# Kernel tuning notes

Hardware: AMD Instinct MI355X
Metric: run time of the kernel (lower is better)

## Reference

```python
import jax, jax.numpy as jnp
import numpy as np

N_WIN = 7
NUM_HEADS = 8
DIM = 256
QK = 256
TOPK = 4
MLP_HID = 4 * DIM
SCALE = QK ** -0.5  # used for both region routing and pixel attention (qk_scale=None)


def _layernorm(x, g, b, eps=1e-6):
    mu = jnp.mean(x, axis=-1, keepdims=True)
    var = jnp.mean(jnp.square(x - mu), axis=-1, keepdims=True)
    return (x - mu) * jax.lax.rsqrt(var + eps) * g + b


def _dwconv(x, w, b):
    # x: NHWC, w: (5,5,1,C) depthwise kernel (torch Conv2d groups=C, padding=2)
    y = jax.lax.conv_general_dilated(
        x, w, window_strides=(1, 1), padding='SAME',
        feature_group_count=x.shape[-1],
        dimension_numbers=('NHWC', 'HWIO', 'NHWC'))
    return y + b


def _bra(x, qkv_w, qkv_b, lepe_w, lepe_b, wo_w, wo_b):
    # BiLevelRoutingAttention, NHWC in/out
    N, H, W, C = x.shape
    j = i = N_WIN
    h, w = H // j, W // i
    p2, w2, m = j * i, h * w, NUM_HEADS
    dq, dv = QK // m, C // m
    # window partition: (N, p2, h, w, C)
    xw = x.reshape(N, j, h, i, w, C).transpose(0, 1, 3, 2, 4, 5).reshape(N, p2, h, w, C)
    qkv = xw @ qkv_w + qkv_b
    q = qkv[..., :QK]            # (N,p2,h,w,QK)
    kv = qkv[..., QK:]           # (N,p2,h,w,QK+C)
    q_pix = q.reshape(N, p2, w2, QK)
    kv_pix = kv.reshape(N, p2, w2, QK + C)
    q_win = jnp.mean(q, axis=(2, 3))                    # (N,p2,QK)
    k_win = jnp.mean(kv[..., :QK], axis=(2, 3))         # (N,p2,QK)
    # LePE: depthwise conv on V in full-image layout
    v_img = kv[..., QK:].reshape(N, j, i, h, w, C).transpose(0, 1, 3, 2, 4, 5).reshape(N, H, W, C)
    lepe = _dwconv(v_img, lepe_w, lepe_b)
    # region-to-region routing, top-k window selection
    logit = jnp.einsum('npc,nqc->npq', q_win * SCALE, k_win)    # (N,p2,p2)
    _, r_idx = jax.lax.top_k(logit, TOPK)                       # (N,p2,TOPK)
    # gather KV of selected windows: (N,p2,TOPK,w2,QK+C)
    kv_sel = kv_pix[jnp.arange(N)[:, None, None], r_idx]
    k_sel = kv_sel[..., :QK].reshape(N, p2, TOPK * w2, m, dq).transpose(0, 1, 3, 2, 4)  # (N,p2,m,kw2,dq)
    v_sel = kv_sel[..., QK:].reshape(N, p2, TOPK * w2, m, dv).transpose(0, 1, 3, 2, 4)  # (N,p2,m,kw2,dv)
    q_h = q_pix.reshape(N, p2, w2, m, dq).transpose(0, 1, 3, 2, 4)                      # (N,p2,m,w2,dq)
    aw = jnp.einsum('npmqd,npmkd->npmqk', q_h * SCALE, k_sel)
    aw = jax.nn.softmax(aw, axis=-1)
    out = jnp.einsum('npmqk,npmkd->npmqd', aw, v_sel)           # (N,p2,m,w2,dv)
    out = out.transpose(0, 1, 3, 2, 4).reshape(N, j, i, h, w, C)
    out = out.transpose(0, 1, 3, 2, 4, 5).reshape(N, H, W, C)
    out = out + lepe
    return out @ wo_w + wo_b


def setup_inputs() -> dict:
    key = jax.random.key(0)
    ks = jax.random.split(key, 8)
    s = 0.02
    return {
        'x': jax.random.normal(ks[0], (8, 56, 56, DIM), dtype=jnp.float32),
        'ln1_g': jnp.ones((DIM,), jnp.float32),
        'ln1_b': jnp.zeros((DIM,), jnp.float32),
        'qkv_w': jax.random.normal(ks[1], (DIM, 2 * QK + DIM), jnp.float32) * s,
        'qkv_b': jnp.zeros((2 * QK + DIM,), jnp.float32),
        'lepe_w': jax.random.normal(ks[2], (5, 5, 1, DIM), jnp.float32) * s,
        'lepe_b': jnp.zeros((DIM,), jnp.float32),
        'wo_w': jax.random.normal(ks[3], (DIM, DIM), jnp.float32) * s,
        'wo_b': jnp.zeros((DIM,), jnp.float32),
        'ln2_g': jnp.ones((DIM,), jnp.float32),
        'ln2_b': jnp.zeros((DIM,), jnp.float32),
        'mlp_w1': jax.random.normal(ks[4], (DIM, MLP_HID), jnp.float32) * s,
        'mlp_b1': jnp.zeros((MLP_HID,), jnp.float32),
        'mlp_w2': jax.random.normal(ks[5], (MLP_HID, DIM), jnp.float32) * s,
        'mlp_b2': jnp.zeros((DIM,), jnp.float32),
    }


def reference(x, ln1_g, ln1_b, qkv_w, qkv_b, lepe_w, lepe_b, wo_w, wo_b,
              ln2_g, ln2_b, mlp_w1, mlp_b1, mlp_w2, mlp_b2):
    x = x + _bra(_layernorm(x, ln1_g, ln1_b), qkv_w, qkv_b, lepe_w, lepe_b, wo_w, wo_b)
    h = _layernorm(x, ln2_g, ln2_b)
    h = jax.nn.gelu(h @ mlp_w1 + mlp_b1, approximate=False) @ mlp_w2 + mlp_b2
    return x + h
```

## Files before the change

kernel.cpp:

```cpp
#include <hip/hip_runtime.h>
#include <hip/hip_bf16.h>

#define NIMG 8
#define HW 56
#define CDIM 256
#define TOK (NIMG*HW*HW)
#define NWIN 49
#define NPW (NIMG*NWIN)
#define ATT_SCALE 0.0625f

typedef __attribute__((ext_vector_type(8))) short short8;
typedef __attribute__((ext_vector_type(4))) short short4v;
typedef __attribute__((ext_vector_type(4))) float f32x4;

static const size_t OFF_WQKV  = 0;
static const size_t OFF_WWO   = 393216;
static const size_t OFF_W1    = 524288;
static const size_t OFF_W2    = 1048576;
static const size_t OFF_XLN   = 1572864;
static const size_t OFF_QKV   = 14417920;
static const size_t OFF_QKWIN = 52953088;
static const size_t OFF_RIDX  = 53755904;
static const size_t OFF_ATTN  = 53762176;
static const size_t OFF_HMID  = OFF_XLN;

__device__ __forceinline__ float gelu_exact(float v) {
    return 0.5f * v * (1.f + erff(v * 0.70710678118654752f));
}
__device__ __forceinline__ short f2bs(float x) {
    __hip_bfloat16 h = __float2bfloat16(x);
    return *(short*)&h;
}
__device__ __forceinline__ float bs2f(short s) {
    return __uint_as_float(((unsigned)(unsigned short)s) << 16);
}
__device__ __forceinline__ void gld16(const short* g, short* l) {
    __builtin_amdgcn_global_load_lds(
        (const __attribute__((address_space(1))) void*)g,
        (__attribute__((address_space(3))) void*)l, 16, 0, 0);
}

__global__ __launch_bounds__(256) void transpose_cast4_k(const float* __restrict__ s0,
                                                         const float* __restrict__ s1,
                                                         const float* __restrict__ s2,
                                                         const float* __restrict__ s3,
                                                         __hip_bfloat16* __restrict__ d0,
                                                         __hip_bfloat16* __restrict__ d1,
                                                         __hip_bfloat16* __restrict__ d2,
                                                         __hip_bfloat16* __restrict__ d3) {
    int b = blockIdx.x;
    const float* src; __hip_bfloat16* dst; int K, N, l;
    if (b < 192)      { src = s0; dst = d0; K = 256;  N = 768;  l = b; }
    else if (b < 256) { src = s1; dst = d1; K = 256;  N = 256;  l = b - 192; }
    else if (b < 512) { src = s2; dst = d2; K = 256;  N = 1024; l = b - 256; }
    else              { src = s3; dst = d3; K = 1024; N = 256;  l = b - 512; }
    int nx = N / 32;
    int n0 = (l % nx) * 32, k0 = (l / nx) * 32;
    __shared__ float t[32][33];
    int tx = threadIdx.x & 31, ty = threadIdx.x >> 5;
    #pragma unroll
    for (int i = 0; i < 32; i += 8)
        t[ty + i][tx] = src[(size_t)(k0 + ty + i) * N + n0 + tx];
    __syncthreads();
    #pragma unroll
    for (int i = 0; i < 32; i += 8)
        dst[(size_t)(n0 + ty + i) * K + k0 + tx] = __float2bfloat16(t[tx][ty + i]);
}

__global__ __launch_bounds__(256) void ln_bf_k(const float* __restrict__ in,
                                               const float* __restrict__ g,
                                               const float* __restrict__ b,
                                               short* __restrict__ out, int remap) {
    int t = blockIdx.x * 4 + (threadIdx.x >> 6);
    int lane = threadIdx.x & 63;
    float4 v = *(const float4*)(in + (size_t)t * 256 + lane * 4);
    float s = v.x + v.y + v.z + v.w;
    float s2 = v.x * v.x + v.y * v.y + v.z * v.z + v.w * v.w;
    #pragma unroll
    for (int o = 32; o > 0; o >>= 1) {
        s  += __shfl_xor(s, o);
        s2 += __shfl_xor(s2, o);
    }
    float mu = s * (1.f / 256.f);
    float rstd = rsqrtf(s2 * (1.f / 256.f) - mu * mu + 1e-6f);
    float4 gv = *(const float4*)(g + lane * 4);
    float4 bv = *(const float4*)(b + lane * 4);
    short4v o;
    o[0] = f2bs((v.x - mu) * rstd * gv.x + bv.x);
    o[1] = f2bs((v.y - mu) * rstd * gv.y + bv.y);
    o[2] = f2bs((v.z - mu) * rstd * gv.z + bv.z);
    o[3] = f2bs((v.w - mu) * rstd * gv.w + bv.w);
    size_t tb;
    if (remap) {
        int n = t / 3136, rem = t % 3136, y = rem / 56, x = rem % 56;
        int p = (y >> 3) * 7 + (x >> 3);
        int si = (y & 7) * 8 + (x & 7);
        tb = (size_t)(n * 49 + p) * 64 + si;
    } else {
        tb = (size_t)t;
    }
    *(short4v*)(out + tb * 256 + lane * 4) = o;
}

__device__ __forceinline__ void mfma_step(const short* As, const short* Bs,
                                          int wm, int wn, int l15, int swr,
                                          f32x4 acc[2][4]) {
    short8 af[2], bfr[4];
    #pragma unroll
    for (int i = 0; i < 2; ++i)
        af[i] = *(const short8*)&As[(wm + i * 16 + l15) * 32 + swr];
    #pragma unroll
    for (int j = 0; j < 4; ++j)
        bfr[j] = *(const short8*)&Bs[(wn + j * 16 + l15) * 32 + swr];
    #pragma unroll
    for (int i = 0; i < 2; ++i)
        #pragma unroll
        for (int j = 0; j < 4; ++j)
            acc[i][j] = __builtin_amdgcn_mfma_f32_16x16x32_bf16(af[i], bfr[j], acc[i][j], 0, 0, 0);
}

template<int MODE>
__global__ __launch_bounds__(256) void gemm64(const short* __restrict__ A,
                                              const short* __restrict__ Bt,
                                              const float* __restrict__ bias,
                                              const float* __restrict__ res,
                                              void* Cv, int M, int N, int K) {
    const int bn = blockIdx.x * 128;
    const int bm = blockIdx.y * 64;
    const int tid = threadIdx.x;
    const int wave = tid >> 6, lane = tid & 63;
    const int l15 = lane & 15, quad = lane >> 4;
    const int wm = (wave & 1) * 32, wn = (wave >> 1) * 64;

    __shared__ __align__(16) short smem[12288];

    f32x4 acc[2][4];
    #pragma unroll
    for (int i = 0; i < 2; ++i)
        #pragma unroll
        for (int j = 0; j < 4; ++j) acc[i][j] = (f32x4){0.f, 0.f, 0.f, 0.f};

    const int crow = lane >> 2;
    const int ckq = ((lane & 3) ^ ((lane >> 3) & 3)) * 8;
    const short* ga  = A  + (size_t)(bm + wave * 16 + crow) * K + ckq;
    const short* gb0 = Bt + (size_t)(bn + wave * 16 + crow) * K + ckq;
    const short* gb1 = gb0 + (size_t)64 * K;
    const int swr = (quad ^ ((l15 >> 1) & 3)) * 8;

    gld16(ga,  smem + wave * 512);
    gld16(gb0, smem + 2048 + wave * 512);
    gld16(gb1, smem + 4096 + wave * 512);
    asm volatile("s_waitcnt vmcnt(0)" ::: "memory");
    __builtin_amdgcn_s_barrier();
    asm volatile("" ::: "memory");

    int cur = 0;
    for (int k0 = 32; k0 < K; k0 += 32) {
        short* nb = smem + (cur ^ 1) * 6144;
        gld16(ga  + k0, nb + wave * 512);
        gld16(gb0 + k0, nb + 2048 + wave * 512);
        gld16(gb1 + k0, nb + 4096 + wave * 512);
        const short* As = smem + cur * 6144;
        mfma_step(As, As + 2048, wm, wn, l15, swr, acc);
        asm volatile("s_waitcnt vmcnt(0) lgkmcnt(0)" ::: "memory");
        __builtin_amdgcn_s_barrier();
        asm volatile("" ::: "memory");
        cur ^= 1;
    }
    {
        const short* As = smem + cur * 6144;
        mfma_step(As, As + 2048, wm, wn, l15, swr, acc);
    }

    if (MODE == 1) {
        #pragma unroll
        for (int i = 0; i < 2; ++i) {
            int row = bm + wm + i * 16 + quad * 4;
            #pragma unroll
            for (int j = 0; j < 4; ++j) {
                int col = bn + wn + j * 16 + l15;
                float bia = bias[col];
                #pragma unroll
                for (int r = 0; r < 4; ++r) {
                    size_t idx = (size_t)(row + r) * N + col;
                    ((float*)Cv)[idx] = acc[i][j][r] + bia + res[idx];
                }
            }
        }
    } else {
        asm volatile("s_waitcnt lgkmcnt(0)" ::: "memory");
        __builtin_amdgcn_s_barrier();
        asm volatile("" ::: "memory");
        float biasv[4];
        #pragma unroll
        for (int j = 0; j < 4; ++j) biasv[j] = bias[bn + wn + j * 16 + l15];
        short* ep = &smem[wave * 1280];
        short* outp = (short*)Cv;
        #pragma unroll
        for (int p = 0; p < 2; ++p) {
            #pragma unroll
            for (int i = 0; i < 2; ++i)
                #pragma unroll
                for (int jj = 0; jj < 2; ++jj) {
                    int j = p * 2 + jj;
                    #pragma unroll
                    for (int r = 0; r < 4; ++r) {
                        float v = acc[i][j][r] + biasv[j];
                        if (MODE == 2) v = gelu_exact(v);
                        ep[(i * 16 + quad * 4 + r) * 40 + jj * 16 + l15] = f2bs(v);
                    }
                }
            __builtin_amdgcn_s_waitcnt(0);
            int c = lane & 3;
            #pragma unroll
            for (int rr = 0; rr < 2; ++rr) {
                int row = rr * 16 + (lane >> 2);
                short8 v = *(const short8*)&ep[row * 40 + c * 8];
                *(short8*)&outp[(size_t)(bm + wm + row) * N + bn + wn + p * 32 + c * 8] = v;
            }
            __builtin_amdgcn_s_waitcnt(0);
        }
    }
}

__global__ __launch_bounds__(256) void win_means_k(const short* __restrict__ qkv,
                                                   float* __restrict__ qkwin) {
    int w = blockIdx.x;
    int cg = (threadIdx.x & 63) * 8;
    int sp = threadIdx.x >> 6;
    float s[8] = {0.f, 0.f, 0.f, 0.f, 0.f, 0.f, 0.f, 0.f};
    const short* base = qkv + (size_t)w * 64 * 768 + cg;
    for (int si = sp; si < 64; si += 4) {
        short8 v = *(const short8*)(base + (size_t)si * 768);
        #pragma unroll
        for (int i = 0; i < 8; ++i) s[i] += bs2f(v[i]);
    }
    __shared__ float red[4][512];
    #pragma unroll
    for (int i = 0; i < 8; ++i) red[sp][cg + i] = s[i];
    __syncthreads();
    for (int c = threadIdx.x; c < 512; c += 256) {
        float t = red[0][c] + red[1][c] + red[2][c] + red[3][c];
        qkwin[(size_t)w * 512 + c] = t * (1.f / 64.f);
    }
}

__global__ __launch_bounds__(64) void route_k(const float* __restrict__ qkwin,
                                              int* __restrict__ ridx) {
    int w = blockIdx.x;
    int n = w / 49;
    int tid = threadIdx.x;
    __shared__ float qv[256];
    __shared__ float lg[49];
    for (int i = tid; i < 256; i += 64) qv[i] = qkwin[(size_t)w * 512 + i] * ATT_SCALE;
    __syncthreads();
    if (tid < 49) {
        const float* kp = qkwin + (size_t)(n * 49 + tid) * 512 + 256;
        float d = 0.f;
        for (int cc = 0; cc < 256; ++cc) d += qv[cc] * kp[cc];
        lg[tid] = d;
    }
    __syncthreads();
    if (tid == 0) {
        #pragma unroll
        for (int t = 0; t < 4; ++t) {
            float best = -1e30f; int bi = 0;
            for (int j = 0; j < 49; ++j)
                if (lg[j] > best) { best = lg[j]; bi = j; }
            lg[bi] = -1e30f;
            ridx[w * 4 + t] = bi;
        }
    }
}

__global__ __launch_bounds__(256) void attn_mfma_k(const short* __restrict__ qkv,
                                                   const int* __restrict__ ridx,
                                                   short* __restrict__ attn) {
    const int blk = blockIdx.x;
    const int w = blk >> 3, h = blk & 7;
    const int n = w / 49;
    const int tid = threadIdx.x;
    const int wave = tid >> 6, lane = tid & 63;
    const int l15 = lane & 15, quad = lane >> 4;

    __shared__ __align__(16) short smem[25344];
    short* Vt = smem;
    short* Ks = smem + 8448;
    short* Ps = smem + 8448;
    __shared__ int rs4[4];
    if (tid < 4) rs4[tid] = ridx[w * 4 + tid];
    __syncthreads();

    {
        int s = tid >> 2, kq = (tid & 3) * 8;
        #pragma unroll
        for (int u = 0; u < 4; ++u) {
            int key = u * 64 + s;
            const short* src = qkv + ((size_t)(n * 49 + rs4[u]) * 64 + s) * 768 + 256 + h * 32 + kq;
            *(short8*)&Ks[key * 40 + kq] = *(const short8*)src;
        }
    }
    {
        int kp = tid & 127, dh = tid >> 7;
        int k0 = kp * 2;
        int t = k0 >> 6, s = k0 & 63;
        const short* src0 = qkv + ((size_t)(n * 49 + rs4[t]) * 64 + s) * 768 + 512 + h * 32 + dh * 16;
        const short* src1 = src0 + 768;
        short8 a0 = *(const short8*)src0, a1 = *(const short8*)(src0 + 8);
        short8 b0 = *(const short8*)src1, b1 = *(const short8*)(src1 + 8);
        #pragma unroll
        for (int d = 0; d < 8; ++d) {
            *(unsigned*)&Vt[(dh * 16 + d) * 264 + k0] =
                (unsigned)(unsigned short)a0[d] | ((unsigned)(unsigned short)b0[d] << 16);
            *(unsigned*)&Vt[(dh * 16 + 8 + d) * 264 + k0] =
                (unsigned)(unsigned short)a1[d] | ((unsigned)(unsigned short)b1[d] << 16);
        }
    }
    __syncthreads();

    const short* qp = qkv + ((size_t)w * 64 + wave * 16 + l15) * 768 + h * 32 + quad * 8;
    short8 qf = *(const short8*)qp;

    f32x4 st[16];
    #pragma unroll
    for (int j = 0; j < 16; ++j) {
        short8 kf = *(const short8*)&Ks[(j * 16 + l15) * 40 + quad * 8];
        st[j] = __builtin_amdgcn_mfma_f32_16x16x32_bf16(kf, qf, (f32x4){0.f, 0.f, 0.f, 0.f}, 0, 0, 0);
    }

    float mx = -1e30f;
    #pragma unroll
    for (int j = 0; j < 16; ++j)
        #pragma unroll
        for (int r = 0; r < 4; ++r) mx = fmaxf(mx, st[j][r]);
    mx = fmaxf(mx, __shfl_xor(mx, 16));
    mx = fmaxf(mx, __shfl_xor(mx, 32));

    __syncthreads();

    short* pw = &Ps[wave * 16 * 264];
    float sum = 0.f;
    #pragma unroll
    for (int j = 0; j < 16; ++j) {
        short4v pv;
        #pragma unroll
        for (int r = 0; r < 4; ++r) {
            float p = __expf((st[j][r] - mx) * ATT_SCALE);
            sum += p;
            pv[r] = f2bs(p);
        }
        *(short4v*)&pw[l15 * 264 + j * 16 + quad * 4] = pv;
    }
    sum += __shfl_xor(sum, 16);
    sum += __shfl_xor(sum, 32);
    float inv = 1.f / sum;
    __builtin_amdgcn_s_waitcnt(0);

    f32x4 oc[2] = {(f32x4){0.f,0.f,0.f,0.f}, (f32x4){0.f,0.f,0.f,0.f}};
    #pragma unroll
    for (int kk = 0; kk < 8; ++kk) {
        short8 pf = *(const short8*)&pw[l15 * 264 + kk * 32 + quad * 8];
        #pragma unroll
        for (int jj = 0; jj < 2; ++jj) {
            short8 vf = *(const short8*)&Vt[(jj * 16 + l15) * 264 + kk * 32 + quad * 8];
            oc[jj] = __builtin_amdgcn_mfma_f32_16x16x32_bf16(vf, pf, oc[jj], 0, 0, 0);
        }
    }

    short* op = attn + ((size_t)w * 64 + wave * 16 + l15) * 256 + h * 32;
    #pragma unroll
    for (int jj = 0; jj < 2; ++jj) {
        short4v o4;
        #pragma unroll
        for (int r = 0; r < 4; ++r) o4[r] = f2bs(oc[jj][r] * inv);
        *(short4v*)&op[jj * 16 + quad * 4] = o4;
    }
}

__global__ __launch_bounds__(256) void lepe_k(const short* __restrict__ qkv,
                                              const short* __restrict__ attn,
                                              const float* __restrict__ lw,
                                              const float* __restrict__ lb,
                                              short* __restrict__ ywo) {
    int t = blockIdx.x * 8 + (threadIdx.x >> 5);
    int c0 = (threadIdx.x & 31) * 8;
    int n = t / 3136, rem = t % 3136, y = rem / 56, x = rem % 56;
    float sum[8];
    {
        float4 b0 = *(const float4*)(lb + c0), b1 = *(const float4*)(lb + c0 + 4);
        sum[0] = b0.x; sum[1] = b0.y; sum[2] = b0.z; sum[3] = b0.w;
        sum[4] = b1.x; sum[5] = b1.y; sum[6] = b1.z; sum[7] = b1.w;
    }
    #pragma unroll
    for (int ky = 0; ky < 5; ++ky) {
        int yy = y + ky - 2;
        if ((unsigned)yy >= 56u) continue;
        #pragma unroll
        for (int kx = 0; kx < 5; ++kx) {
            int xx = x + kx - 2;
            if ((unsigned)xx >= 56u) continue;
            int p = (yy >> 3) * 7 + (xx >> 3);
            int si = (yy & 7) * 8 + (xx & 7);
            short8 v = *(const short8*)(qkv + ((size_t)(n * 49 + p) * 64 + si) * 768 + 512 + c0);
            const float* wp = lw + (ky * 5 + kx) * 256 + c0;
            float4 w0 = *(const float4*)wp, w1 = *(const float4*)(wp + 4);
            sum[0] += bs2f(v[0]) * w0.x; sum[1] += bs2f(v[1]) * w0.y;
            sum[2] += bs2f(v[2]) * w0.z; sum[3] += bs2f(v[3]) * w0.w;
            sum[4] += bs2f(v[4]) * w1.x; sum[5] += bs2f(v[5]) * w1.y;
            sum[6] += bs2f(v[6]) * w1.z; sum[7] += bs2f(v[7]) * w1.w;
        }
    }
    int p0 = (y >> 3) * 7 + (x >> 3);
    int s0 = (y & 7) * 8 + (x & 7);
    short8 a = *(const short8*)(attn + ((size_t)(n * 49 + p0) * 64 + s0) * 256 + c0);
    short8 o;
    #pragma unroll
    for (int i = 0; i < 8; ++i) o[i] = f2bs(sum[i] + bs2f(a[i]));
    *(short8*)(ywo + (size_t)t * 256 + c0) = o;
}

extern "C" void kernel_launch(void* const* d_in, const int* in_sizes, int n_in,
                              void* d_out, int out_size, void* d_ws, size_t ws_size,
                              hipStream_t stream) {
    const float* x      = (const float*)d_in[0];
    const float* ln1_g  = (const float*)d_in[1];
    const float* ln1_b  = (const float*)d_in[2];
    const float* qkv_w  = (const float*)d_in[3];
    const float* qkv_b  = (const float*)d_in[4];
    const float* lepe_w = (const float*)d_in[5];
    const float* lepe_b = (const float*)d_in[6];
    const float* wo_w   = (const float*)d_in[7];
    const float* wo_b   = (const float*)d_in[8];
    const float* ln2_g  = (const float*)d_in[9];
    const float* ln2_b  = (const float*)d_in[10];
    const float* mlp_w1 = (const float*)d_in[11];
    const float* mlp_b1 = (const float*)d_in[12];
    const float* mlp_w2 = (const float*)d_in[13];
    const float* mlp_b2 = (const float*)d_in[14];
    float* out = (float*)d_out;

    char* ws = (char*)d_ws;
    __hip_bfloat16* wqkvT = (__hip_bfloat16*)(ws + OFF_WQKV);
    __hip_bfloat16* wwoT  = (__hip_bfloat16*)(ws + OFF_WWO);
    __hip_bfloat16* w1T   = (__hip_bfloat16*)(ws + OFF_W1);
    __hip_bfloat16* w2T   = (__hip_bfloat16*)(ws + OFF_W2);
    short* xln   = (short*)(ws + OFF_XLN);
    short* qkvb  = (short*)(ws + OFF_QKV);
    float* qkwin = (float*)(ws + OFF_QKWIN);
    int*   ridx  = (int*)(ws + OFF_RIDX);
    short* attnb = (short*)(ws + OFF_ATTN);
    short* ywo   = (short*)(ws + OFF_XLN);
    short* h2    = (short*)(ws + OFF_ATTN);
    short* hmid  = (short*)(ws + OFF_HMID);

    transpose_cast4_k<<<768, 256, 0, stream>>>(qkv_w, wo_w, mlp_w1, mlp_w2,
                                               wqkvT, wwoT, w1T, w2T);
    ln_bf_k<<<TOK/4, 256, 0, stream>>>(x, ln1_g, ln1_b, xln, 1);
    gemm64<0><<<dim3(6, 392), 256, 0, stream>>>(xln, (const short*)wqkvT,
                                                qkv_b, nullptr, qkvb, TOK, 768, 256);
    win_means_k<<<NPW, 256, 0, stream>>>(qkvb, qkwin);
    route_k<<<NPW, 64, 0, stream>>>(qkwin, ridx);
    attn_mfma_k<<<NPW * 8, 256, 0, stream>>>(qkvb, ridx, attnb);
    lepe_k<<<TOK/8, 256, 0, stream>>>(qkvb, attnb, lepe_w, lepe_b, ywo);
    gemm64<1><<<dim3(2, 392), 256, 0, stream>>>(ywo, (const short*)wwoT,
                                                wo_b, x, out, TOK, 256, 256);
    ln_bf_k<<<TOK/4, 256, 0, stream>>>(out, ln2_g, ln2_b, h2, 0);
    gemm64<2><<<dim3(8, 392), 256, 0, stream>>>(h2, (const short*)w1T,
                                                mlp_b1, nullptr, hmid, TOK, 1024, 256);
    gemm64<1><<<dim3(2, 392), 256, 0, stream>>>(hmid, (const short*)w2T,
                                                mlp_b2, out, out, TOK, 256, 1024);
}
```

Measured before the change: 299.7 us.

## Fuse window means into QKV GEMM and use 2-wave 64x128 GEMM tiles

The GEMM kernel now runs with 128 threads (2 waves), and each wave computes a full 64x64 sub-tile, giving a 4x4 MFMA accumulator per wave instead of 2x4. The QKV GEMM epilogue computes per-window column means of q and k directly from the fp32 accumulators, since each 64-row block is exactly one window. This removes the separate win_means kernel and its re-read of the qkv buffer. In exchange, per-thread register use rises, fewer waves are resident per block, and the means now come from fp32 accumulators rather than from bf16-rounded values.

```diff
diff --git a/kernel.cpp b/kernel.cpp
--- a/kernel.cpp
+++ b/kernel.cpp
@@ -102,66 +102,79 @@
     *(short4v*)(out + tb * 256 + lane * 4) = o;
 }
 
-__device__ __forceinline__ void mfma_step(const short* As, const short* Bs,
-                                          int wm, int wn, int l15, int swr,
-                                          f32x4 acc[2][4]) {
-    short8 af[2], bfr[4];
-    #pragma unroll
-    for (int i = 0; i < 2; ++i)
-        af[i] = *(const short8*)&As[(wm + i * 16 + l15) * 32 + swr];
+__device__ __forceinline__ void mfma_step64(const short* As, const short* Bs,
+                                            int wn, int l15, int swr,
+                                            f32x4 acc[4][4]) {
+    short8 af[4], bfr[4];
+    #pragma unroll
+    for (int i = 0; i < 4; ++i)
+        af[i] = *(const short8*)&As[(i * 16 + l15) * 32 + swr];
     #pragma unroll
     for (int j = 0; j < 4; ++j)
         bfr[j] = *(const short8*)&Bs[(wn + j * 16 + l15) * 32 + swr];
     #pragma unroll
-    for (int i = 0; i < 2; ++i)
+    for (int i = 0; i < 4; ++i)
         #pragma unroll
         for (int j = 0; j < 4; ++j)
             acc[i][j] = __builtin_amdgcn_mfma_f32_16x16x32_bf16(af[i], bfr[j], acc[i][j], 0, 0, 0);
 }
 
 template<int MODE>
-__global__ __launch_bounds__(256) void gemm64(const short* __restrict__ A,
+__global__ __launch_bounds__(128) void gemm64(const short* __restrict__ A,
                                               const short* __restrict__ Bt,
                                               const float* __restrict__ bias,
                                               const float* __restrict__ res,
-                                              void* Cv, int M, int N, int K) {
+                                              void* Cv, float* __restrict__ winptr,
+                                              int M, int N, int K) {
     const int bn = blockIdx.x * 128;
     const int bm = blockIdx.y * 64;
     const int tid = threadIdx.x;
     const int wave = tid >> 6, lane = tid & 63;
     const int l15 = lane & 15, quad = lane >> 4;
-    const int wm = (wave & 1) * 32, wn = (wave >> 1) * 64;
+    const int wn = wave * 64;
 
     __shared__ __align__(16) short smem[12288];
 
-    f32x4 acc[2][4];
-    #pragma unroll
-    for (int i = 0; i < 2; ++i)
+    f32x4 acc[4][4];
+    #pragma unroll
+    for (int i = 0; i < 4; ++i)
         #pragma unroll
         for (int j = 0; j < 4; ++j) acc[i][j] = (f32x4){0.f, 0.f, 0.f, 0.f};
 
-    const int crow = lane >> 2;
-    const int ckq = ((lane & 3) ^ ((lane >> 3) & 3)) * 8;
-    const short* ga  = A  + (size_t)(bm + wave * 16 + crow) * K + ckq;
-    const short* gb0 = Bt + (size_t)(bn + wave * 16 + crow) * K + ckq;
-    const short* gb1 = gb0 + (size_t)64 * K;
+    const int srow = lane >> 2;
+    const int scg  = ((lane & 3) ^ ((lane >> 3) & 3)) * 8;
+    const short* ga0 = A  + (size_t)(bm + wave * 16 + srow) * K + scg;
+    const short* ga1 = ga0 + (size_t)32 * K;
+    const short* gb0 = Bt + (size_t)(bn + wave * 16 + srow) * K + scg;
+    const short* gb1 = gb0 + (size_t)32 * K;
+    const short* gb2 = gb0 + (size_t)64 * K;
+    const short* gb3 = gb0 + (size_t)96 * K;
     const int swr = (quad ^ ((l15 >> 1) & 3)) * 8;
 
-    gld16(ga,  smem + wave * 512);
-    gld16(gb0, smem + 2048 + wave * 512);
-    gld16(gb1, smem + 4096 + wave * 512);
+    {
+        short* b = smem;
+        gld16(ga0, b + wave * 512);
+        gld16(ga1, b + (2 + wave) * 512);
+        gld16(gb0, b + 2048 + wave * 512);
+        gld16(gb1, b + 2048 + (2 + wave) * 512);
+        gld16(gb2, b + 2048 + (4 + wave) * 512);
+        gld16(gb3, b + 2048 + (6 + wave) * 512);
+    }
     asm volatile("s_waitcnt vmcnt(0)" ::: "memory");
     __builtin_amdgcn_s_barrier();
     asm volatile("" ::: "memory");
 
     int cur = 0;
     for (int k0 = 32; k0 < K; k0 += 32) {
-        short* nb = smem + (cur ^ 1) * 6144;
-        gld16(ga  + k0, nb + wave * 512);
-        gld16(gb0 + k0, nb + 2048 + wave * 512);
-        gld16(gb1 + k0, nb + 4096 + wave * 512);
+        short* b = smem + (cur ^ 1) * 6144;
+        gld16(ga0 + k0, b + wave * 512);
+        gld16(ga1 + k0, b + (2 + wave) * 512);
+        gld16(gb0 + k0, b + 2048 + wave * 512);
+        gld16(gb1 + k0, b + 2048 + (2 + wave) * 512);
+        gld16(gb2 + k0, b + 2048 + (4 + wave) * 512);
+        gld16(gb3 + k0, b + 2048 + (6 + wave) * 512);
         const short* As = smem + cur * 6144;
-        mfma_step(As, As + 2048, wm, wn, l15, swr, acc);
+        mfma_step64(As, As + 2048, wn, l15, swr, acc);
         asm volatile("s_waitcnt vmcnt(0) lgkmcnt(0)" ::: "memory");
         __builtin_amdgcn_s_barrier();
         asm volatile("" ::: "memory");
@@ -169,13 +182,32 @@
     }
     {
         const short* As = smem + cur * 6144;
-        mfma_step(As, As + 2048, wm, wn, l15, swr, acc);
+        mfma_step64(As, As + 2048, wn, l15, swr, acc);
+    }
+
+    if (MODE == 0) {
+        if (bn + wn < 512) {
+            #pragma unroll
+            for (int j = 0; j < 4; ++j) {
+                float s = 0.f;
+                #pragma unroll
+                for (int i = 0; i < 4; ++i)
+                    #pragma unroll
+                    for (int r = 0; r < 4; ++r) s += acc[i][j][r];
+                s += __shfl_xor(s, 16);
+                s += __shfl_xor(s, 32);
+                if (quad == 0) {
+                    int col = bn + wn + j * 16 + l15;
+                    winptr[(size_t)blockIdx.y * 512 + col] = s * (1.f / 64.f) + bias[col];
+                }
+            }
+        }
     }
 
     if (MODE == 1) {
         #pragma unroll
-        for (int i = 0; i < 2; ++i) {
-            int row = bm + wm + i * 16 + quad * 4;
+        for (int i = 0; i < 4; ++i) {
+            int row = bm + i * 16 + quad * 4;
             #pragma unroll
             for (int j = 0; j < 4; ++j) {
                 int col = bn + wn + j * 16 + l15;
@@ -197,51 +229,32 @@
         short* ep = &smem[wave * 1280];
         short* outp = (short*)Cv;
         #pragma unroll
-        for (int p = 0; p < 2; ++p) {
+        for (int ii = 0; ii < 2; ++ii) {
             #pragma unroll
-            for (int i = 0; i < 2; ++i)
+            for (int p = 0; p < 2; ++p) {
                 #pragma unroll
-                for (int jj = 0; jj < 2; ++jj) {
-                    int j = p * 2 + jj;
+                for (int i = 0; i < 2; ++i)
                     #pragma unroll
-                    for (int r = 0; r < 4; ++r) {
-                        float v = acc[i][j][r] + biasv[j];
-                        if (MODE == 2) v = gelu_exact(v);
-                        ep[(i * 16 + quad * 4 + r) * 40 + jj * 16 + l15] = f2bs(v);
+                    for (int jj = 0; jj < 2; ++jj) {
+                        int j = p * 2 + jj;
+                        #pragma unroll
+                        for (int r = 0; r < 4; ++r) {
+                            float v = acc[ii * 2 + i][j][r] + biasv[j];
+                            if (MODE == 2) v = gelu_exact(v);
+                            ep[(i * 16 + quad * 4 + r) * 40 + jj * 16 + l15] = f2bs(v);
+                        }
                     }
+                __builtin_amdgcn_s_waitcnt(0);
+                int c = lane & 3;
+                #pragma unroll
+                for (int rr = 0; rr < 2; ++rr) {
+                    int row = rr * 16 + (lane >> 2);
+                    short8 v = *(const short8*)&ep[row * 40 + c * 8];
+                    *(short8*)&outp[(size_t)(bm + ii * 32 + row) * N + bn + wn + p * 32 + c * 8] = v;
                 }
-            __builtin_amdgcn_s_waitcnt(0);
-            int c = lane & 3;
-            #pragma unroll
-            for (int rr = 0; rr < 2; ++rr) {
-                int row = rr * 16 + (lane >> 2);
-                short8 v = *(const short8*)&ep[row * 40 + c * 8];
-                *(short8*)&outp[(size_t)(bm + wm + row) * N + bn + wn + p * 32 + c * 8] = v;
+                __builtin_amdgcn_s_waitcnt(0);
             }
-            __builtin_amdgcn_s_waitcnt(0);
-        }
-    }
-}
-
-__global__ __launch_bounds__(256) void win_means_k(const short* __restrict__ qkv,
-                                                   float* __restrict__ qkwin) {
-    int w = blockIdx.x;
-    int cg = (threadIdx.x & 63) * 8;
-    int sp = threadIdx.x >> 6;
-    float s[8] = {0.f, 0.f, 0.f, 0.f, 0.f, 0.f, 0.f, 0.f};
-    const short* base = qkv + (size_t)w * 64 * 768 + cg;
-    for (int si = sp; si < 64; si += 4) {
-        short8 v = *(const short8*)(base + (size_t)si * 768);
-        #pragma unroll
-        for (int i = 0; i < 8; ++i) s[i] += bs2f(v[i]);
-    }
-    __shared__ float red[4][512];
-    #pragma unroll
-    for (int i = 0; i < 8; ++i) red[sp][cg + i] = s[i];
-    __syncthreads();
-    for (int c = threadIdx.x; c < 512; c += 256) {
-        float t = red[0][c] + red[1][c] + red[2][c] + red[3][c];
-        qkwin[(size_t)w * 512 + c] = t * (1.f / 64.f);
+        }
     }
 }
 
@@ -456,17 +469,16 @@
     transpose_cast4_k<<<768, 256, 0, stream>>>(qkv_w, wo_w, mlp_w1, mlp_w2,
                                                wqkvT, wwoT, w1T, w2T);
     ln_bf_k<<<TOK/4, 256, 0, stream>>>(x, ln1_g, ln1_b, xln, 1);
-    gemm64<0><<<dim3(6, 392), 256, 0, stream>>>(xln, (const short*)wqkvT,
-                                                qkv_b, nullptr, qkvb, TOK, 768, 256);
-    win_means_k<<<NPW, 256, 0, stream>>>(qkvb, qkwin);
+    gemm64<0><<<dim3(6, 392), 128, 0, stream>>>(xln, (const short*)wqkvT,
+                                                qkv_b, nullptr, qkvb, qkwin, TOK, 768, 256);
     route_k<<<NPW, 64, 0, stream>>>(qkwin, ridx);
     attn_mfma_k<<<NPW * 8, 256, 0, stream>>>(qkvb, ridx, attnb);
     lepe_k<<<TOK/8, 256, 0, stream>>>(qkvb, attnb, lepe_w, lepe_b, ywo);
-    gemm64<1><<<dim3(2, 392), 256, 0, stream>>>(ywo, (const short*)wwoT,
-                                                wo_b, x, out, TOK, 256, 256);
+    gemm64<1><<<dim3(2, 392), 128, 0, stream>>>(ywo, (const short*)wwoT,
+                                                wo_b, x, out, nullptr, TOK, 256, 256);
     ln_bf_k<<<TOK/4, 256, 0, stream>>>(out, ln2_g, ln2_b, h2, 0);
-    gemm64<2><<<dim3(8, 392), 256, 0, stream>>>(h2, (const short*)w1T,
-                                                mlp_b1, nullptr, hmid, TOK, 1024, 256);
-    gemm64<1><<<dim3(2, 392), 256, 0, stream>>>(hmid, (const short*)w2T,
-                                                mlp_b2, out, out, TOK, 256, 1024);
-}
+    gemm64<2><<<dim3(8, 392), 128, 0, stream>>>(h2, (const short*)w1T,
+                                                mlp_b1, nullptr, hmid, nullptr, TOK, 1024, 256);
+    gemm64<1><<<dim3(2, 392), 128, 0, stream>>>(hmid, (const short*)w2T,
+                                                mlp_b2, out, out, nullptr, TOK, 256, 1024);
+}
```

Result: slower. 328.4 us (+9.6%).

## Fuse window means into QKV GEMM epilogue and triple-buffer GEMM loads

Applied to the files above, without the earlier changes.

The per-window query/key mean reduction is computed from the QKV GEMM accumulators in the epilogue, since each 64-row tile is exactly one window, removing the separate win_means kernel and its re-read of the QKV buffer. The GEMM main loop is changed to triple-buffered LDS with two tiles in flight and partial vmcnt waits. Shared memory grows to 36KB per block, which may lower occupancy, and means are now taken on fp32 values before bf16 rounding.

```diff
diff --git a/kernel.cpp b/kernel.cpp
--- a/kernel.cpp
+++ b/kernel.cpp
@@ -124,7 +124,8 @@
                                               const short* __restrict__ Bt,
                                               const float* __restrict__ bias,
                                               const float* __restrict__ res,
-                                              void* Cv, int M, int N, int K) {
+                                              void* Cv, float* __restrict__ winptr,
+                                              int M, int N, int K) {
     const int bn = blockIdx.x * 128;
     const int bm = blockIdx.y * 64;
     const int tid = threadIdx.x;
@@ -132,7 +133,7 @@
     const int l15 = lane & 15, quad = lane >> 4;
     const int wm = (wave & 1) * 32, wn = (wave >> 1) * 64;
 
-    __shared__ __align__(16) short smem[12288];
+    __shared__ __align__(16) short smem[18432];
 
     f32x4 acc[2][4];
     #pragma unroll
@@ -140,36 +141,66 @@
         #pragma unroll
         for (int j = 0; j < 4; ++j) acc[i][j] = (f32x4){0.f, 0.f, 0.f, 0.f};
 
-    const int crow = lane >> 2;
-    const int ckq = ((lane & 3) ^ ((lane >> 3) & 3)) * 8;
-    const short* ga  = A  + (size_t)(bm + wave * 16 + crow) * K + ckq;
-    const short* gb0 = Bt + (size_t)(bn + wave * 16 + crow) * K + ckq;
+    const int srow = lane >> 2;
+    const int scg  = ((lane & 3) ^ ((lane >> 3) & 3)) * 8;
+    const short* ga  = A  + (size_t)(bm + wave * 16 + srow) * K + scg;
+    const short* gb0 = Bt + (size_t)(bn + wave * 16 + srow) * K + scg;
     const short* gb1 = gb0 + (size_t)64 * K;
     const int swr = (quad ^ ((l15 >> 1) & 3)) * 8;
 
-    gld16(ga,  smem + wave * 512);
-    gld16(gb0, smem + 2048 + wave * 512);
-    gld16(gb1, smem + 4096 + wave * 512);
-    asm volatile("s_waitcnt vmcnt(0)" ::: "memory");
-    __builtin_amdgcn_s_barrier();
-    asm volatile("" ::: "memory");
-
-    int cur = 0;
-    for (int k0 = 32; k0 < K; k0 += 32) {
-        short* nb = smem + (cur ^ 1) * 6144;
-        gld16(ga  + k0, nb + wave * 512);
-        gld16(gb0 + k0, nb + 2048 + wave * 512);
-        gld16(gb1 + k0, nb + 4096 + wave * 512);
-        const short* As = smem + cur * 6144;
-        mfma_step(As, As + 2048, wm, wn, l15, swr, acc);
-        asm volatile("s_waitcnt vmcnt(0) lgkmcnt(0)" ::: "memory");
+    const int nt = K >> 5;
+
+    {
+        short* b0 = smem;
+        gld16(ga,       b0 + wave * 512);
+        gld16(gb0,      b0 + 2048 + wave * 512);
+        gld16(gb1,      b0 + 4096 + wave * 512);
+        short* b1 = smem + 6144;
+        gld16(ga  + 32, b1 + wave * 512);
+        gld16(gb0 + 32, b1 + 2048 + wave * 512);
+        gld16(gb1 + 32, b1 + 4096 + wave * 512);
+    }
+
+    for (int t = 0; t < nt; ++t) {
+        if (t == nt - 1) asm volatile("s_waitcnt vmcnt(0)" ::: "memory");
+        else             asm volatile("s_waitcnt vmcnt(3)" ::: "memory");
         __builtin_amdgcn_s_barrier();
         asm volatile("" ::: "memory");
-        cur ^= 1;
-    }
-    {
-        const short* As = smem + cur * 6144;
+        if (t + 2 < nt) {
+            short* b = smem + ((t + 2) % 3) * 6144;
+            int kk = (t + 2) * 32;
+            gld16(ga  + kk, b + wave * 512);
+            gld16(gb0 + kk, b + 2048 + wave * 512);
+            gld16(gb1 + kk, b + 4096 + wave * 512);
+        }
+        const short* As = smem + (t % 3) * 6144;
         mfma_step(As, As + 2048, wm, wn, l15, swr, acc);
+    }
+
+    if (MODE == 0) {
+        if (bn < 512) {
+            float* wmean = (float*)&smem[12288];
+            #pragma unroll
+            for (int j = 0; j < 4; ++j) {
+                float s = 0.f;
+                #pragma unroll
+                for (int i = 0; i < 2; ++i)
+                    #pragma unroll
+                    for (int r = 0; r < 4; ++r) s += acc[i][j][r];
+                s += __shfl_xor(s, 16);
+                s += __shfl_xor(s, 32);
+                if (quad == 0) wmean[wave * 64 + j * 16 + l15] = s;
+            }
+            __syncthreads();
+            if (tid < 128) {
+                int c = tid;
+                float s = (c < 64) ? (wmean[c] + wmean[64 + c])
+                                   : (wmean[64 + c] + wmean[128 + c]);
+                int col = bn + c;
+                if (col < 512)
+                    winptr[(size_t)blockIdx.y * 512 + col] = s * (1.f / 64.f) + bias[col];
+            }
+        }
     }
 
     if (MODE == 1) {
@@ -223,28 +254,6 @@
     }
 }
 
-__global__ __launch_bounds__(256) void win_means_k(const short* __restrict__ qkv,
-                                                   float* __restrict__ qkwin) {
-    int w = blockIdx.x;
-    int cg = (threadIdx.x & 63) * 8;
-    int sp = threadIdx.x >> 6;
-    float s[8] = {0.f, 0.f, 0.f, 0.f, 0.f, 0.f, 0.f, 0.f};
-    const short* base = qkv + (size_t)w * 64 * 768 + cg;
-    for (int si = sp; si < 64; si += 4) {
-        short8 v = *(const short8*)(base + (size_t)si * 768);
-        #pragma unroll
-        for (int i = 0; i < 8; ++i) s[i] += bs2f(v[i]);
-    }
-    __shared__ float red[4][512];
-    #pragma unroll
-    for (int i = 0; i < 8; ++i) red[sp][cg + i] = s[i];
-    __syncthreads();
-    for (int c = threadIdx.x; c < 512; c += 256) {
-        float t = red[0][c] + red[1][c] + red[2][c] + red[3][c];
-        qkwin[(size_t)w * 512 + c] = t * (1.f / 64.f);
-    }
-}
-
 __global__ __launch_bounds__(64) void route_k(const float* __restrict__ qkwin,
                                               int* __restrict__ ridx) {
     int w = blockIdx.x;
@@ -457,16 +466,15 @@
                                                wqkvT, wwoT, w1T, w2T);
     ln_bf_k<<<TOK/4, 256, 0, stream>>>(x, ln1_g, ln1_b, xln, 1);
     gemm64<0><<<dim3(6, 392), 256, 0, stream>>>(xln, (const short*)wqkvT,
-                                                qkv_b, nullptr, qkvb, TOK, 768, 256);
-    win_means_k<<<NPW, 256, 0, stream>>>(qkvb, qkwin);
+                                                qkv_b, nullptr, qkvb, qkwin, TOK, 768, 256);
     route_k<<<NPW, 64, 0, stream>>>(qkwin, ridx);
     attn_mfma_k<<<NPW * 8, 256, 0, stream>>>(qkvb, ridx, attnb);
     lepe_k<<<TOK/8, 256, 0, stream>>>(qkvb, attnb, lepe_w, lepe_b, ywo);
     gemm64<1><<<dim3(2, 392), 256, 0, stream>>>(ywo, (const short*)wwoT,
-                                                wo_b, x, out, TOK, 256, 256);
+                                                wo_b, x, out, nullptr, TOK, 256, 256);
     ln_bf_k<<<TOK/4, 256, 0, stream>>>(out, ln2_g, ln2_b, h2, 0);
     gemm64<2><<<dim3(8, 392), 256, 0, stream>>>(h2, (const short*)w1T,
-                                                mlp_b1, nullptr, hmid, TOK, 1024, 256);
+                                                mlp_b1, nullptr, hmid, nullptr, TOK, 1024, 256);
     gemm64<1><<<dim3(2, 392), 256, 0, stream>>>(hmid, (const short*)w2T,
-                                                mlp_b2, out, out, TOK, 256, 1024);
-}
+                                                mlp_b2, out, out, nullptr, TOK, 256, 1024);
+}
```

New measurement: 293.6 us. 1.02x faster.
